# Performance work log

Measured on AMD Instinct MI355X. Metric: run time of the kernel, lower is better.

Reference implementation:

```python
import jax, jax.numpy as jnp
import numpy as np
import math

RADIUS2 = 0.1 * 0.1   # QueryAndGroup(0.1, 64)
NSAMPLE = 64
NEG_SLOPE = 0.2


def get_lattice_points(b, n):
    # AtlasNet-style regular UV grid in [0,1]^2, first n points of a ceil(sqrt(n))^2 grid
    side = int(math.ceil(math.sqrt(n)))
    u = jnp.linspace(0.0, 1.0, side, dtype=jnp.float32)
    gx, gy = jnp.meshgrid(u, u, indexing='ij')
    pts = jnp.stack([gx.ravel(), gy.ravel()], axis=-1)[:n]  # (n, 2)
    return jnp.broadcast_to(pts[None], (b, n, 2))


def conv1x1(x, W, b):
    # 1x1 Conv1d == per-point GEMM: x (B,Cin,N), W (Cout,Cin), b (Cout,)
    return jnp.einsum('oc,bcn->bon', W, x) + b[None, :, None]


def mlp(x, params):
    for W, b in params:
        x = jax.nn.leaky_relu(conv1x1(x, W, b), NEG_SLOPE)
    return x


def ball_group_max(points, feats):
    # points (B,N,3), feats (B,C,N). Ball query (radius 0.1, first 64 in index
    # order, pad with first hit) + feature gather + max over neighborhood.
    B, N, _ = points.shape
    sq = jnp.sum(points * points, axis=-1)  # (B,N)
    d2 = sq[:, :, None] + sq[:, None, :] - 2.0 * jnp.einsum('bnd,bmd->bnm', points, points)
    mask = d2 < RADIUS2                                    # (B,N,N)
    cand = jnp.where(mask, jnp.arange(N, dtype=jnp.int32)[None, None, :], N)
    idx = jnp.sort(cand, axis=-1)[:, :, :NSAMPLE]          # first NSAMPLE hits
    first = idx[:, :, :1]
    idx = jnp.where(idx == N, first, idx)                  # pad with first hit (self always hits)
    idx = jnp.minimum(idx, N - 1)
    ft = jnp.swapaxes(feats, 1, 2)                         # (B,N,C)
    gathered = ft[jnp.arange(B)[:, None, None], idx]       # (B,N,K,C)
    return jnp.swapaxes(gathered.max(axis=2), 1, 2)        # (B,C,N)


def setup_inputs() -> dict:
    key = jax.random.key(0)
    ks = jax.random.split(key, 20)
    s = 0.05
    inp = {
        'z':   jax.random.normal(ks[0], (2, 512), dtype=jnp.float32),
        'W1a': jax.random.normal(ks[1], (512, 514), dtype=jnp.float32) * s,
        'b1a': jnp.zeros((512,), jnp.float32),
        'W1b': jax.random.normal(ks[2], (512, 512), dtype=jnp.float32) * s,
        'b1b': jnp.zeros((512,), jnp.float32),
        'W1c': jax.random.normal(ks[3], (512, 512), dtype=jnp.float32) * s,
        'b1c': jnp.zeros((512,), jnp.float32),
        'Wx1': jax.random.normal(ks[4], (3, 512), dtype=jnp.float32) * s,
        'bx1': jnp.zeros((3,), jnp.float32),
        'W2a': jax.random.normal(ks[5], (512, 1536), dtype=jnp.float32) * s,
        'b2a': jnp.zeros((512,), jnp.float32),
        'W2b': jax.random.normal(ks[6], (512, 512), dtype=jnp.float32) * s,
        'b2b': jnp.zeros((512,), jnp.float32),
        'W2c': jax.random.normal(ks[7], (512, 512), dtype=jnp.float32) * s,
        'b2c': jnp.zeros((512,), jnp.float32),
        'Wx2': jax.random.normal(ks[8], (3, 512), dtype=jnp.float32) * s,
        'bx2': jnp.zeros((3,), jnp.float32),
        'n1': 1024,
        'n2': 2048,
    }
    return inp


def reference(z, W1a, b1a, W1b, b1b, W1c, b1c, Wx1, bx1,
              W2a, b2a, W2b, b2b, W2c, b2c, Wx2, bx2, n1, n2):
    B, dim = z.shape

    def stage1(n):
        latt = get_lattice_points(B, n)                                    # (B,n,2)
        zc = jnp.concatenate([jnp.broadcast_to(z[:, None, :], (B, n, dim)), latt], axis=2)
        x = jnp.swapaxes(zc, 1, 2)                                         # (B,514,n)
        h = mlp(x, [(W1a, b1a), (W1b, b1b), (W1c, b1c)])                   # (B,512,n)
        pts = jnp.swapaxes(jax.nn.sigmoid(conv1x1(h, Wx1, bx1)), 1, 2) - 0.5
        return h, pts

    _, first_stage_points = stage1(n1)
    h2, fine_points = stage1(n2)

    local = ball_group_max(fine_points, h2)                                # (B,512,n2)
    glob = jnp.broadcast_to(h2.max(axis=2, keepdims=True), h2.shape)       # (B,512,n2)
    feat = jnp.concatenate([h2, local, glob], axis=1)                      # (B,1536,n2)

    f = mlp(feat, [(W2a, b2a), (W2b, b2b), (W2c, b2c)])
    delta = 0.1 * (jax.nn.sigmoid(conv1x1(f, Wx2, bx2)) - 0.5)
    second_stage_points = jnp.swapaxes(delta, 1, 2) + fine_points
    return (first_stage_points, second_stage_points, fine_points)
```

## Files before the change

### kernel.cpp

```cpp
#include <hip/hip_runtime.h>
#include <math.h>

#define B 2
#define N1 1024
#define N2 2048
#define R1TOT 6144
#define R2TOT 4096
#define SLOPE 0.2f

typedef short bf16x8 __attribute__((ext_vector_type(8)));
typedef float f32x4 __attribute__((ext_vector_type(4)));
typedef unsigned short u16x4 __attribute__((ext_vector_type(4)));
typedef unsigned short u16x8 __attribute__((ext_vector_type(8)));

__device__ __forceinline__ unsigned short f2bf(float x) {
    unsigned int u = __float_as_uint(x);
    unsigned int r = (u + 0x7fffu + ((u >> 16) & 1u)) >> 16;
    return (unsigned short)r;
}
__device__ __forceinline__ float bf2f(unsigned short h) {
    return __uint_as_float(((unsigned int)h) << 16);
}
__device__ __forceinline__ unsigned fenc(float f) {
    unsigned u = __float_as_uint(f);
    return (u & 0x80000000u) ? ~u : (u | 0x80000000u);
}
__device__ __forceinline__ float fdec(unsigned u) {
    unsigned b = (u & 0x80000000u) ? (u & 0x7FFFFFFFu) : ~u;
    return __uint_as_float(b);
}

#define OFF_WP     0
#define OFF_X1P    6291456
#define OFF_XMP    18874368
#define OFF_X2P    31457280
#define OFF_X3P    39845888
#define OFF_X4P    44040192
#define OFF_C1     48234496
#define OFF_GLOBE  48238592
#define OFF_GBIAS  48242688
#define OFF_HACC1  48246784
#define OFF_HACC2  48345088
#define ZERO_WORDS 43008

__global__ void k_prep(const float* __restrict__ W1b, const float* __restrict__ W1c,
                       const float* __restrict__ W2b, const float* __restrict__ W2c,
                       const float* __restrict__ W2a, unsigned short* __restrict__ wp,
                       const float* __restrict__ z, const float* __restrict__ W1a,
                       const float* __restrict__ b1a, float* __restrict__ c1,
                       float* __restrict__ zbase) {
    int bx = blockIdx.x, tid = threadIdx.x;
    if (bx < 6144) {
        int idx = bx * 256 + tid;
        const float* src; unsigned short* dst; int o, k, K, in_ld;
        if (idx < 1048576) {
            int which = idx >> 18; int local = idx & 262143;
            K = 512; in_ld = 512;
            src = (which == 0) ? W1b : (which == 1) ? W1c : (which == 2) ? W2b : W2c;
            dst = wp + (long)which * 524288;
            o = local >> 9; k = local & 511;
        } else {
            int local = idx - 1048576;
            K = 1024; in_ld = 1536; src = W2a; dst = wp + 2097152;
            o = local >> 10; k = local & 1023;
        }
        float v = src[(long)o * in_ld + k];
        unsigned short hi = f2bf(v);
        dst[(long)o * 2 * K + k] = hi;
        dst[(long)o * 2 * K + K + k] = f2bf(v - bf2f(hi));
    } else if (bx < 6152) {
        for (int l = (bx - 6144) * 256 + tid; l < ZERO_WORDS; l += 2048) zbase[l] = 0.f;
    } else {
        int gid = (bx - 6152) * 4 + (tid >> 6);
        int lane = tid & 63;
        int b = gid >> 9, o = gid & 511;
        float acc = 0.f;
        const float* wr = W1a + (long)o * 514;
        const float* zb = z + b * 512;
        for (int k = lane; k < 512; k += 64) acc += wr[k] * zb[k];
        #pragma unroll
        for (int off = 32; off > 0; off >>= 1) acc += __shfl_down(acc, off, 64);
        if (lane == 0) c1[gid] = acc + b1a[o];
    }
}

__global__ void k_layer_a(const float* __restrict__ W1a, const float* __restrict__ c1,
                          unsigned short* __restrict__ X1) {
    int bx = blockIdx.x;
    int r = bx >> 1;
    int o = ((bx & 1) << 8) + threadIdx.x;
    int b, n, side;
    if (r < 2048) { b = r >> 10; n = r & 1023; side = 32; }
    else          { int r2 = r - 2048; b = r2 >> 11; n = r2 & 2047; side = 46; }
    int row, col;
    if (side == 32) { row = n >> 5; col = n & 31; }
    else            { row = n / 46; col = n - row * 46; }
    double inv = 1.0 / (double)(side - 1);
    float lx = (row == side - 1) ? 1.0f : (float)(row * inv);
    float ly = (col == side - 1) ? 1.0f : (float)(col * inv);
    float h = c1[b * 512 + o] + W1a[(long)o * 514 + 512] * lx + W1a[(long)o * 514 + 513] * ly;
    h = (h > 0.f) ? h : SLOPE * h;
    unsigned short hi = f2bf(h);
    X1[(long)r * 1024 + o] = hi;
    X1[(long)r * 1024 + 512 + o] = f2bf(h - bf2f(hi));
}

template<int TERMS>
__global__ __launch_bounds__(256, (TERMS == 3) ? 3 : 4) void k_gemm(
    const unsigned short* __restrict__ Wp, int ldw,
    const unsigned short* __restrict__ Xp, int ldx,
    int K,
    const float* __restrict__ bias, int bias_div,
    unsigned short* __restrict__ Xn, int ldxn, int lo_off, int row_off, int pack_min,
    const float* __restrict__ Wx, float* __restrict__ hacc,
    unsigned* __restrict__ globE, int glob_min) {

    constexpr int NBUF  = (TERMS == 3) ? 1 : 2;
    constexpr int BUFSZ = (TERMS == 3) ? 32768 : 16384;
    constexpr int XBASE = (TERMS == 3) ? 16384 : 8192;
    __shared__ __align__(16) char sm[NBUF * BUFSZ];

    const int t = threadIdx.x;
    const int nb0 = blockIdx.x * 64;
    const int ob0 = blockIdx.y * 64;

    const unsigned short* gp[8];
    int lo_[8];
    #pragma unroll
    for (int p = 0; p < 8; ++p) {
        const int T = p >> 1;
        if (TERMS == 1 && (T == 1 || T == 3)) continue;
        int j2 = ((p & 1) << 8) + t;
        int r = j2 >> 3, cl = j2 & 7, cs = cl ^ (r & 7);
        gp[p] = (T < 2)
            ? (Wp + (long)(ob0 + r) * ldw + ((T == 1) ? K : 0) + cs * 8)
            : (Xp + (long)(nb0 + r) * ldx + ((T == 3) ? K : 0) + cs * 8);
        const int reg = (TERMS == 3) ? p : ((p < 2) ? p : p - 2);
        lo_[p] = reg * 4096 + t * 16;
    }

    const int lane = t & 63, w = t >> 6;
    const int wy = w >> 1, wx = w & 1;
    const int quad = lane >> 4, l15 = lane & 15;
    const int xm = l15 & 7;
    const int rowA = (wy * 32 + l15) * 128;
    const int rowB = (wx * 32 + l15) * 128;
    const int ca0 = (quad ^ xm) * 16;
    const int ca1 = ((quad + 4) ^ xm) * 16;

    f32x4 acc[2][2];
    #pragma unroll
    for (int i = 0; i < 2; ++i)
        #pragma unroll
        for (int j = 0; j < 2; ++j) { f32x4 zz = {0.f, 0.f, 0.f, 0.f}; acc[i][j] = zz; }

    auto stage = [&](int buf, int k0) {
        #pragma unroll
        for (int p = 0; p < 8; ++p) {
            const int T = p >> 1;
            if (TERMS == 1 && (T == 1 || T == 3)) continue;
            __builtin_amdgcn_global_load_lds(
                (const __attribute__((address_space(1))) void*)(const void*)(gp[p] + k0),
                (__attribute__((address_space(3))) void*)(void*)(sm + buf * BUFSZ + lo_[p]),
                16, 0, 0);
        }
    };

    auto compute = [&](int buf) {
        char* smb = sm + buf * BUFSZ;
        #pragma unroll
        for (int sub = 0; sub < 2; ++sub) {
            const int cb = (sub == 0) ? ca0 : ca1;
            bf16x8 ah[2], bh[2];
            #pragma unroll
            for (int i = 0; i < 2; ++i)
                ah[i] = *(const bf16x8*)(const void*)(smb + rowA + i * 2048 + cb);
            #pragma unroll
            for (int j = 0; j < 2; ++j)
                bh[j] = *(const bf16x8*)(const void*)(smb + XBASE + rowB + j * 2048 + cb);
            if (TERMS == 3) {
                bf16x8 al[2], bl[2];
                #pragma unroll
                for (int i = 0; i < 2; ++i)
                    al[i] = *(const bf16x8*)(const void*)(smb + 8192 + rowA + i * 2048 + cb);
                #pragma unroll
                for (int j = 0; j < 2; ++j)
                    bl[j] = *(const bf16x8*)(const void*)(smb + 24576 + rowB + j * 2048 + cb);
                #pragma unroll
                for (int i = 0; i < 2; ++i)
                    #pragma unroll
                    for (int j = 0; j < 2; ++j) {
                        acc[i][j] = __builtin_amdgcn_mfma_f32_16x16x32_bf16(ah[i], bh[j], acc[i][j], 0, 0, 0);
                        acc[i][j] = __builtin_amdgcn_mfma_f32_16x16x32_bf16(ah[i], bl[j], acc[i][j], 0, 0, 0);
                        acc[i][j] = __builtin_amdgcn_mfma_f32_16x16x32_bf16(al[i], bh[j], acc[i][j], 0, 0, 0);
                    }
            } else {
                #pragma unroll
                for (int i = 0; i < 2; ++i)
                    #pragma unroll
                    for (int j = 0; j < 2; ++j)
                        acc[i][j] = __builtin_amdgcn_mfma_f32_16x16x32_bf16(ah[i], bh[j], acc[i][j], 0, 0, 0);
            }
        }
    };

    if constexpr (TERMS == 3) {
        for (int k0 = 0; k0 < K; k0 += 64) {
            stage(0, k0);
            __syncthreads();
            compute(0);
            __syncthreads();
        }
    } else {
        stage(0, 0);
        __syncthreads();
        int cur = 0;
        for (int k0 = 64; k0 < K; k0 += 64) {
            stage(cur ^ 1, k0);
            compute(cur);
            __syncthreads();
            cur ^= 1;
        }
        compute(cur);
    }

    float val[2][2][4];
    #pragma unroll
    for (int j = 0; j < 2; ++j) {
        int n = nb0 + wx * 32 + j * 16 + l15;
        int bidx0 = (bias_div >= (1 << 29)) ? 0 : (n / bias_div) * 512;
        #pragma unroll
        for (int i = 0; i < 2; ++i) {
            int ob = ob0 + wy * 32 + i * 16 + quad * 4;
            #pragma unroll
            for (int r = 0; r < 4; ++r) {
                float x = acc[i][j][r] + bias[bidx0 + ob + r];
                val[i][j][r] = (x > 0.f) ? x : SLOPE * x;
            }
        }
        if (Xn && n >= pack_min) {
            long nl = n - row_off;
            #pragma unroll
            for (int i = 0; i < 2; ++i) {
                int ob = ob0 + wy * 32 + i * 16 + quad * 4;
                u16x4 h4;
                #pragma unroll
                for (int r = 0; r < 4; ++r) h4[r] = f2bf(val[i][j][r]);
                *(u16x4*)(void*)(Xn + nl * ldxn + ob) = h4;
                if (lo_off) {
                    u16x4 l4;
                    #pragma unroll
                    for (int r = 0; r < 4; ++r) l4[r] = f2bf(val[i][j][r] - bf2f(h4[r]));
                    *(u16x4*)(void*)(Xn + nl * ldxn + lo_off + ob) = l4;
                }
            }
        }
    }

    if (hacc) {
        __syncthreads();
        float* smh = (float*)sm;
        unsigned* smg = (unsigned*)(sm + 1024);
        if (t < 256) smh[t] = 0.f;
        if (t < 64) smg[t] = 0u;
        __syncthreads();
        float wxv[3][2][4];
        #pragma unroll
        for (int ch = 0; ch < 3; ++ch)
            #pragma unroll
            for (int i = 0; i < 2; ++i)
                #pragma unroll
                for (int r = 0; r < 4; ++r)
                    wxv[ch][i][r] = Wx[ch * 512 + ob0 + wy * 32 + i * 16 + quad * 4 + r];
        #pragma unroll
        for (int j = 0; j < 2; ++j) {
            int nl = wx * 32 + j * 16 + l15;
            float p0 = 0.f, p1 = 0.f, p2 = 0.f;
            #pragma unroll
            for (int i = 0; i < 2; ++i)
                #pragma unroll
                for (int r = 0; r < 4; ++r) {
                    float v = val[i][j][r];
                    p0 += v * wxv[0][i][r];
                    p1 += v * wxv[1][i][r];
                    p2 += v * wxv[2][i][r];
                }
            atomicAdd(&smh[nl * 4 + 0], p0);
            atomicAdd(&smh[nl * 4 + 1], p1);
            atomicAdd(&smh[nl * 4 + 2], p2);
        }
        if (globE && nb0 >= glob_min) {
            #pragma unroll
            for (int i = 0; i < 2; ++i)
                #pragma unroll
                for (int r = 0; r < 4; ++r) {
                    float mx = fmaxf(val[i][0][r], val[i][1][r]);
                    atomicMax(&smg[wy * 32 + i * 16 + quad * 4 + r], fenc(mx));
                }
        }
        __syncthreads();
        if (t < 64) {
            atomicAdd(&hacc[(long)(nb0 + t) * 4 + 0], smh[t * 4 + 0]);
            atomicAdd(&hacc[(long)(nb0 + t) * 4 + 1], smh[t * 4 + 1]);
            atomicAdd(&hacc[(long)(nb0 + t) * 4 + 2], smh[t * 4 + 2]);
            if (globE && nb0 >= glob_min) {
                int b = (nb0 - glob_min) >> 11;
                atomicMax(&globE[b * 512 + ob0 + t], smg[t]);
            }
        }
    }
}

__global__ void k_finalize(const float* __restrict__ bx1, const float* __restrict__ hacc1,
                           float* __restrict__ out0, float* __restrict__ out2,
                           const float* __restrict__ W2a, const float* __restrict__ b2a,
                           const unsigned* __restrict__ globE, float* __restrict__ gbias) {
    int bx = blockIdx.x, tid = threadIdx.x;
    if (bx < 24) {
        int r = bx * 256 + tid;
        float* dst = (r < 2048) ? (out0 + (long)r * 3) : (out2 + (long)(r - 2048) * 3);
        #pragma unroll
        for (int ch = 0; ch < 3; ++ch) {
            float a = hacc1[(long)r * 4 + ch] + bx1[ch];
            dst[ch] = 1.f / (1.f + expf(-a)) - 0.5f;
        }
    } else {
        int gid = (bx - 24) * 4 + (tid >> 6);
        int lane = tid & 63;
        int b = gid >> 9, o = gid & 511;
        float acc = 0.f;
        const float* wr = W2a + (long)o * 1536 + 1024;
        for (int k = lane; k < 512; k += 64) acc += wr[k] * fdec(globE[b * 512 + k]);
        #pragma unroll
        for (int off = 32; off > 0; off >>= 1) acc += __shfl_down(acc, off, 64);
        if (lane == 0) gbias[gid] = acc + b2a[o];
    }
}

__global__ __launch_bounds__(256) void k_ball(const float* __restrict__ fine,
                                              unsigned short* __restrict__ X2P) {
    int i = blockIdx.x, b = blockIdx.y;
    int tid = threadIdx.x, lane = tid & 63, wv = tid >> 6;
    __shared__ int idxl[64];
    __shared__ int wcnt[4];
    __shared__ float part[8][256];
    const float* fb = fine + (long)b * N2 * 3;
    float xi = fb[i * 3 + 0], yi = fb[i * 3 + 1], zi = fb[i * 3 + 2];
    float sqi = __fadd_rn(__fadd_rn(__fmul_rn(xi, xi), __fmul_rn(yi, yi)), __fmul_rn(zi, zi));
    int cnt = 0;
    for (int it = 0; it < N2 / 256; ++it) {
        int j = it * 256 + tid;
        float xj = fb[j * 3 + 0], yj = fb[j * 3 + 1], zj = fb[j * 3 + 2];
        float sqj = __fadd_rn(__fadd_rn(__fmul_rn(xj, xj), __fmul_rn(yj, yj)), __fmul_rn(zj, zj));
        float dot = __fadd_rn(__fadd_rn(__fmul_rn(xi, xj), __fmul_rn(yi, yj)), __fmul_rn(zi, zj));
        float d2 = __fsub_rn(__fadd_rn(sqi, sqj), __fmul_rn(2.0f, dot));
        bool pred = d2 < 0.01f;
        unsigned long long m = __ballot(pred);
        if (lane == 0) wcnt[wv] = __popcll(m);
        __syncthreads();
        int wbase = cnt;
        #pragma unroll
        for (int q = 0; q < 3; ++q) { if (q < wv) wbase += wcnt[q]; }
        int total = wcnt[0] + wcnt[1] + wcnt[2] + wcnt[3];
        int rank = wbase + __popcll(m & ((1ull << lane) - 1ull));
        if (pred && rank < 64) idxl[rank] = j;
        cnt += total;
        if (cnt >= 64) break;
        __syncthreads();
    }
    __syncthreads();
    int m = min(cnt, 64);

    const unsigned short* hb = X2P + (long)b * N2 * 1024;
    int g = tid & 63, q = tid >> 6;
    float mx[8];
    #pragma unroll
    for (int r = 0; r < 8; ++r) mx[r] = -1e30f;
    for (int jj = q; jj < m; jj += 4) {
        u16x8 v = *(const u16x8*)(const void*)(hb + (long)idxl[jj] * 1024 + g * 8);
        #pragma unroll
        for (int r = 0; r < 8; ++r) mx[r] = fmaxf(mx[r], bf2f(v[r]));
    }
    #pragma unroll
    for (int r = 0; r < 8; ++r) part[r][tid] = mx[r];
    __syncthreads();
    if (tid < 64) {
        unsigned short* orow = X2P + (long)(b * N2 + i) * 1024;
        u16x8 hi;
        #pragma unroll
        for (int r = 0; r < 8; ++r) {
            float v0 = fmaxf(fmaxf(part[r][tid], part[r][tid + 64]),
                             fmaxf(part[r][tid + 128], part[r][tid + 192]));
            hi[r] = (unsigned short)(__float_as_uint(v0) >> 16);
        }
        *(u16x8*)(void*)(orow + 512 + tid * 8) = hi;
    }
}

__global__ void k_final2(const float* __restrict__ bx2, const float* __restrict__ hacc2,
                         const float* __restrict__ fine, float* __restrict__ out1) {
    int r = blockIdx.x * 256 + threadIdx.x;
    #pragma unroll
    for (int ch = 0; ch < 3; ++ch) {
        float a = hacc2[(long)r * 4 + ch] + bx2[ch];
        out1[(long)r * 3 + ch] = fine[(long)r * 3 + ch] + 0.1f * (1.f / (1.f + expf(-a)) - 0.5f);
    }
}

extern "C" void kernel_launch(void* const* d_in, const int* in_sizes, int n_in,
                              void* d_out, int out_size, void* d_ws, size_t ws_size,
                              hipStream_t stream) {
    const float* z   = (const float*)d_in[0];
    const float* W1a = (const float*)d_in[1];
    const float* b1a = (const float*)d_in[2];
    const float* W1b = (const float*)d_in[3];
    const float* b1b = (const float*)d_in[4];
    const float* W1c = (const float*)d_in[5];
    const float* b1c = (const float*)d_in[6];
    const float* Wx1 = (const float*)d_in[7];
    const float* bx1 = (const float*)d_in[8];
    const float* W2a = (const float*)d_in[9];
    const float* b2a = (const float*)d_in[10];
    const float* W2b = (const float*)d_in[11];
    const float* b2b = (const float*)d_in[12];
    const float* W2c = (const float*)d_in[13];
    const float* b2c = (const float*)d_in[14];
    const float* Wx2 = (const float*)d_in[15];
    const float* bx2 = (const float*)d_in[16];

    char* wsb = (char*)d_ws;
    unsigned short* WP   = (unsigned short*)(wsb + OFF_WP);
    unsigned short* X1P  = (unsigned short*)(wsb + OFF_X1P);
    unsigned short* XMP  = (unsigned short*)(wsb + OFF_XMP);
    unsigned short* X2P  = (unsigned short*)(wsb + OFF_X2P);
    unsigned short* X3P  = (unsigned short*)(wsb + OFF_X3P);
    unsigned short* X4P  = (unsigned short*)(wsb + OFF_X4P);
    float*    c1    = (float*)(wsb + OFF_C1);
    unsigned* globE = (unsigned*)(wsb + OFF_GLOBE);
    float*    gbias = (float*)(wsb + OFF_GBIAS);
    float*    hacc1 = (float*)(wsb + OFF_HACC1);
    float*    hacc2 = (float*)(wsb + OFF_HACC2);

    unsigned short* WP1b = WP;
    unsigned short* WP1c = WP + 524288;
    unsigned short* WP2b = WP + 1048576;
    unsigned short* WP2c = WP + 1572864;
    unsigned short* WP2a = WP + 2097152;

    float* out0 = (float*)d_out;
    float* out1 = out0 + B * N1 * 3;
    float* out2 = out1 + B * N2 * 3;
    float* fine = out2;

    const int BIG = 1 << 30;

    k_prep<<<6408, 256, 0, stream>>>(W1b, W1c, W2b, W2c, W2a, WP, z, W1a, b1a, c1,
                                     (float*)(wsb + OFF_GLOBE));
    k_layer_a<<<12288, 256, 0, stream>>>(W1a, c1, X1P);

    k_gemm<3><<<dim3(96, 8), 256, 0, stream>>>(WP1b, 1024, X1P, 1024, 512, b1b, BIG,
                                               XMP, 1024, 512, 0, 0,
                                               nullptr, nullptr, nullptr, 0);
    k_gemm<3><<<dim3(96, 8), 256, 0, stream>>>(WP1c, 1024, XMP, 1024, 512, b1c, BIG,
                                               X2P, 1024, 0, 2048, 2048,
                                               Wx1, hacc1, globE, 2048);
    k_finalize<<<280, 256, 0, stream>>>(bx1, hacc1, out0, out2, W2a, b2a, globE, gbias);
    k_ball<<<dim3(N2, B), 256, 0, stream>>>(fine, X2P);

    k_gemm<1><<<dim3(64, 8), 256, 0, stream>>>(WP2a, 2048, X2P, 1024, 1024, gbias, 2048,
                                               X3P, 512, 0, 0, 0,
                                               nullptr, nullptr, nullptr, 0);
    k_gemm<1><<<dim3(64, 8), 256, 0, stream>>>(WP2b, 1024, X3P, 512, 512, b2b, BIG,
                                               X4P, 512, 0, 0, 0,
                                               nullptr, nullptr, nullptr, 0);
    k_gemm<1><<<dim3(64, 8), 256, 0, stream>>>(WP2c, 1024, X4P, 512, 512, b2c, BIG,
                                               nullptr, 0, 0, 0, 0,
                                               Wx2, hacc2, nullptr, 0);
    k_final2<<<16, 256, 0, stream>>>(bx2, hacc2, fine, out1);
}
```

Baseline: 205.6 us.

## Batch eight ball-query centers per block and deduplicate neighbor gathers

The ball-query kernel now handles eight consecutive query points per block. It stages all points in shared memory and marks each candidate with a per-query bitmask, so each distinct neighbor row is gathered once and max-reduced into every query that selected it. This cuts redundant global reads of the 512-channel feature rows shared by nearby queries, at the cost of more registers, more shared memory and an atomic-built unique list. Separately, the weight prep kernel skips writing the bf16 low-residual halves for weights whose GEMMs use only the high part.

```diff
diff --git a/kernel.cpp b/kernel.cpp
--- a/kernel.cpp
+++ b/kernel.cpp
@@ -7,6 +7,7 @@
 #define R1TOT 6144
 #define R2TOT 4096
 #define SLOPE 0.2f
+#define QG 8
 
 typedef short bf16x8 __attribute__((ext_vector_type(8)));
 typedef float f32x4 __attribute__((ext_vector_type(4)));
@@ -53,21 +54,25 @@
     if (bx < 6144) {
         int idx = bx * 256 + tid;
         const float* src; unsigned short* dst; int o, k, K, in_ld;
+        bool need_lo;
         if (idx < 1048576) {
             int which = idx >> 18; int local = idx & 262143;
             K = 512; in_ld = 512;
             src = (which == 0) ? W1b : (which == 1) ? W1c : (which == 2) ? W2b : W2c;
             dst = wp + (long)which * 524288;
             o = local >> 9; k = local & 511;
+            need_lo = (which < 2);
         } else {
             int local = idx - 1048576;
             K = 1024; in_ld = 1536; src = W2a; dst = wp + 2097152;
             o = local >> 10; k = local & 1023;
+            need_lo = false;
         }
         float v = src[(long)o * in_ld + k];
         unsigned short hi = f2bf(v);
         dst[(long)o * 2 * K + k] = hi;
-        dst[(long)o * 2 * K + K + k] = f2bf(v - bf2f(hi));
+        if (need_lo)
+            dst[(long)o * 2 * K + K + k] = f2bf(v - bf2f(hi));
     } else if (bx < 6152) {
         for (int l = (bx - 6144) * 256 + tid; l < ZERO_WORDS; l += 2048) zbase[l] = 0.f;
     } else {
@@ -337,63 +342,119 @@
     }
 }
 
-__global__ __launch_bounds__(256) void k_ball(const float* __restrict__ fine,
-                                              unsigned short* __restrict__ X2P) {
-    int i = blockIdx.x, b = blockIdx.y;
+__global__ __launch_bounds__(256, 4) void k_ball(const float* __restrict__ fine,
+                                                 unsigned short* __restrict__ X2P) {
+    int i0 = blockIdx.x * QG, b = blockIdx.y;
     int tid = threadIdx.x, lane = tid & 63, wv = tid >> 6;
-    __shared__ int idxl[64];
-    __shared__ int wcnt[4];
-    __shared__ float part[8][256];
+    __shared__ float pts[N2 * 3];
+    __shared__ unsigned char mark[N2];
+    __shared__ int wcnt[4][QG];
+    __shared__ int ulist[512];
+    __shared__ int ucnt;
+    __shared__ float part4[4][512];
+
     const float* fb = fine + (long)b * N2 * 3;
-    float xi = fb[i * 3 + 0], yi = fb[i * 3 + 1], zi = fb[i * 3 + 2];
-    float sqi = __fadd_rn(__fadd_rn(__fmul_rn(xi, xi), __fmul_rn(yi, yi)), __fmul_rn(zi, zi));
-    int cnt = 0;
+    for (int l = tid; l < N2 * 3; l += 256) pts[l] = fb[l];
+    *(int*)(void*)&mark[tid * 8] = 0;
+    *(int*)(void*)&mark[tid * 8 + 4] = 0;
+    if (tid == 0) ucnt = 0;
+    __syncthreads();
+
+    float cx[QG], cy[QG], cz[QG], sqc[QG];
+    #pragma unroll
+    for (int g = 0; g < QG; ++g) {
+        cx[g] = pts[(i0 + g) * 3 + 0];
+        cy[g] = pts[(i0 + g) * 3 + 1];
+        cz[g] = pts[(i0 + g) * 3 + 2];
+        sqc[g] = __fadd_rn(__fadd_rn(__fmul_rn(cx[g], cx[g]), __fmul_rn(cy[g], cy[g])),
+                           __fmul_rn(cz[g], cz[g]));
+    }
+
+    int cnt[QG];
+    #pragma unroll
+    for (int g = 0; g < QG; ++g) cnt[g] = 0;
+
     for (int it = 0; it < N2 / 256; ++it) {
         int j = it * 256 + tid;
-        float xj = fb[j * 3 + 0], yj = fb[j * 3 + 1], zj = fb[j * 3 + 2];
+        float xj = pts[j * 3 + 0], yj = pts[j * 3 + 1], zj = pts[j * 3 + 2];
         float sqj = __fadd_rn(__fadd_rn(__fmul_rn(xj, xj), __fmul_rn(yj, yj)), __fmul_rn(zj, zj));
-        float dot = __fadd_rn(__fadd_rn(__fmul_rn(xi, xj), __fmul_rn(yi, yj)), __fmul_rn(zi, zj));
-        float d2 = __fsub_rn(__fadd_rn(sqi, sqj), __fmul_rn(2.0f, dot));
-        bool pred = d2 < 0.01f;
-        unsigned long long m = __ballot(pred);
-        if (lane == 0) wcnt[wv] = __popcll(m);
-        __syncthreads();
-        int wbase = cnt;
-        #pragma unroll
-        for (int q = 0; q < 3; ++q) { if (q < wv) wbase += wcnt[q]; }
-        int total = wcnt[0] + wcnt[1] + wcnt[2] + wcnt[3];
-        int rank = wbase + __popcll(m & ((1ull << lane) - 1ull));
-        if (pred && rank < 64) idxl[rank] = j;
-        cnt += total;
-        if (cnt >= 64) break;
-        __syncthreads();
+        unsigned long long bm[QG];
+        #pragma unroll
+        for (int g = 0; g < QG; ++g) {
+            float dot = __fadd_rn(__fadd_rn(__fmul_rn(cx[g], xj), __fmul_rn(cy[g], yj)),
+                                  __fmul_rn(cz[g], zj));
+            float d2 = __fsub_rn(__fadd_rn(sqc[g], sqj), __fmul_rn(2.0f, dot));
+            bm[g] = __ballot(d2 < 0.01f);
+        }
+        if (lane < QG) wcnt[wv][lane] = __popcll(bm[lane]);
+        __syncthreads();
+        unsigned mybits = 0;
+        #pragma unroll
+        for (int g = 0; g < QG; ++g) {
+            int base = cnt[g];
+            #pragma unroll
+            for (int q = 0; q < 3; ++q) { if (q < wv) base += wcnt[q][g]; }
+            int rank = base + __popcll(bm[g] & ((1ull << lane) - 1ull));
+            if (((bm[g] >> lane) & 1ull) && rank < 64) mybits |= 1u << g;
+            cnt[g] += wcnt[0][g] + wcnt[1][g] + wcnt[2][g] + wcnt[3][g];
+        }
+        mark[j] = (unsigned char)mybits;
+        bool done = true;
+        #pragma unroll
+        for (int g = 0; g < QG; ++g) done = done && (cnt[g] >= 64);
+        __syncthreads();
+        if (done) break;
+    }
+
+    for (int it = 0; it < N2 / 256; ++it) {
+        int j = it * 256 + tid;
+        unsigned mk = mark[j];
+        if (mk) { int r = atomicAdd(&ucnt, 1); ulist[r] = j | ((int)mk << 16); }
     }
     __syncthreads();
-    int m = min(cnt, 64);
+    int nu = ucnt;
 
     const unsigned short* hb = X2P + (long)b * N2 * 1024;
-    int g = tid & 63, q = tid >> 6;
-    float mx[8];
-    #pragma unroll
-    for (int r = 0; r < 8; ++r) mx[r] = -1e30f;
-    for (int jj = q; jj < m; jj += 4) {
-        u16x8 v = *(const u16x8*)(const void*)(hb + (long)idxl[jj] * 1024 + g * 8);
-        #pragma unroll
-        for (int r = 0; r < 8; ++r) mx[r] = fmaxf(mx[r], bf2f(v[r]));
-    }
-    #pragma unroll
-    for (int r = 0; r < 8; ++r) part[r][tid] = mx[r];
-    __syncthreads();
-    if (tid < 64) {
-        unsigned short* orow = X2P + (long)(b * N2 + i) * 1024;
-        u16x8 hi;
-        #pragma unroll
-        for (int r = 0; r < 8; ++r) {
-            float v0 = fmaxf(fmaxf(part[r][tid], part[r][tid + 64]),
-                             fmaxf(part[r][tid + 128], part[r][tid + 192]));
-            hi[r] = (unsigned short)(__float_as_uint(v0) >> 16);
-        }
-        *(u16x8*)(void*)(orow + 512 + tid * 8) = hi;
+    int cl = tid & 63, q = tid >> 6;
+    float acc[QG][8];
+    #pragma unroll
+    for (int g = 0; g < QG; ++g)
+        #pragma unroll
+        for (int r = 0; r < 8; ++r) acc[g][r] = -1e30f;
+    for (int u = q; u < nu; u += 4) {
+        int e = ulist[u];
+        int j = e & 0xFFFF;
+        unsigned mk = ((unsigned)e) >> 16;
+        u16x8 v = *(const u16x8*)(const void*)(hb + (long)j * 1024 + cl * 8);
+        float f[8];
+        #pragma unroll
+        for (int r = 0; r < 8; ++r) f[r] = bf2f(v[r]);
+        #pragma unroll
+        for (int g = 0; g < QG; ++g) {
+            if (mk & (1u << g)) {
+                #pragma unroll
+                for (int r = 0; r < 8; ++r) acc[g][r] = fmaxf(acc[g][r], f[r]);
+            }
+        }
+    }
+
+    #pragma unroll 1
+    for (int g = 0; g < QG; ++g) {
+        __syncthreads();
+        #pragma unroll
+        for (int r = 0; r < 8; ++r) part4[q][cl * 8 + r] = acc[g][r];
+        __syncthreads();
+        if (tid < 64) {
+            unsigned short* orow = X2P + (long)(b * N2 + i0 + g) * 1024;
+            u16x8 hi;
+            #pragma unroll
+            for (int r = 0; r < 8; ++r) {
+                float v0 = fmaxf(fmaxf(part4[0][tid * 8 + r], part4[1][tid * 8 + r]),
+                                 fmaxf(part4[2][tid * 8 + r], part4[3][tid * 8 + r]));
+                hi[r] = (unsigned short)(__float_as_uint(v0) >> 16);
+            }
+            *(u16x8*)(void*)(orow + 512 + tid * 8) = hi;
+        }
     }
 }
 
@@ -465,7 +526,7 @@
                                                X2P, 1024, 0, 2048, 2048,
                                                Wx1, hacc1, globE, 2048);
     k_finalize<<<280, 256, 0, stream>>>(bx1, hacc1, out0, out2, W2a, b2a, globE, gbias);
-    k_ball<<<dim3(N2, B), 256, 0, stream>>>(fine, X2P);
+    k_ball<<<dim3(N2 / QG, B), 256, 0, stream>>>(fine, X2P);
 
     k_gemm<1><<<dim3(64, 8), 256, 0, stream>>>(WP2a, 2048, X2P, 1024, 1024, gbias, 2048,
                                                X3P, 512, 0, 0, 0,
```

After: 262.3 us. +27.6%, slower.
